# Performance work log

Hardware: AMD Instinct MI355X
Metric: run time of the kernel (lower is better)

## Reference

```python
import jax, jax.numpy as jnp
import numpy as np

N_NODES = 100000
N_EDGES = 1600000
D_IN = 128
D_OUT = 128


def setup_inputs() -> dict:
    key = jax.random.key(0)
    k_x, k_w, k_r, k_c, k_v = jax.random.split(key, 5)
    x = jax.random.normal(k_x, (N_NODES, D_IN), dtype=jnp.float32)
    # xavier_uniform: U(-a, a), a = sqrt(6/(fan_in+fan_out))
    a = float(np.sqrt(6.0 / (D_IN + D_OUT)))
    W = jax.random.uniform(k_w, (D_IN, D_OUT), dtype=jnp.float32, minval=-a, maxval=a)
    edge_row = jax.random.randint(k_r, (N_EDGES,), 0, N_NODES, dtype=jnp.int32)
    edge_col = jax.random.randint(k_c, (N_EDGES,), 0, N_NODES, dtype=jnp.int32)
    edge_val = jax.random.uniform(k_v, (N_EDGES,), dtype=jnp.float32)
    return {"x": x, "W": W, "edge_row": edge_row, "edge_col": edge_col, "edge_val": edge_val}


def reference(x, W, edge_row, edge_col, edge_val):
    # dropout with p=0.0 is the identity (module default), so omitted.
    support = x @ W                                  # [N, D_OUT] dense GEMM
    # sparse adj @ support in COO form: out[r] += v * support[c]
    msgs = support[edge_col] * edge_val[:, None]      # [E, D_OUT] irregular gather
    out = jax.ops.segment_sum(msgs, edge_row, num_segments=x.shape[0])
    return jnp.tanh(out)
```

## Files before the change

kernel.cpp:

```cpp
#include <hip/hip_runtime.h>
#include <hip/hip_bf16.h>
#include <hip/hip_fp16.h>
#include <math.h>

#define D 128
#define BIN_SHIFT 8
#define BIN_ROWS 256
#define NB_MAX 512
#define CPAD 16
#define AW 4096

typedef _Float16 half8 __attribute__((ext_vector_type(8)));
typedef float floatx4 __attribute__((ext_vector_type(4)));
typedef float floatx2 __attribute__((ext_vector_type(2)));

__global__ void gcn_wt_kernel(const float* __restrict__ W,
                              unsigned short* __restrict__ wt,
                              int* __restrict__ cbin) {
    const int i = blockIdx.x * 256 + threadIdx.x;
    const int n = i >> 7, k = i & 127;
    wt[i] = __half_as_ushort(__float2half_rn(W[k * D + n]));
    if (blockIdx.x < 2) cbin[blockIdx.x * 256 + threadIdx.x] = 0;
}

__global__ __launch_bounds__(256) void gcn_gemm_kernel(
        const float* __restrict__ x, const unsigned short* __restrict__ wt,
        unsigned short* __restrict__ support2, int n_nodes) {
    const int wave = threadIdx.x >> 6;
    const int lane = threadIdx.x & 63;
    const int q = lane >> 4;
    const int n16 = lane & 15;
    const int row_base = blockIdx.x * 128 + wave * 32;
    if (row_base >= n_nodes) return;

    const half8* wt8 = (const half8*)wt;

    floatx4 acc[2][8];
#pragma unroll
    for (int mt = 0; mt < 2; ++mt)
#pragma unroll
        for (int nt = 0; nt < 8; ++nt) acc[mt][nt] = (floatx4){0.f, 0.f, 0.f, 0.f};

#pragma unroll
    for (int kc = 0; kc < 4; ++kc) {
        half8 b[8];
#pragma unroll
        for (int nt = 0; nt < 8; ++nt)
            b[nt] = wt8[(nt * 16 + n16) * 16 + kc * 4 + q];
#pragma unroll
        for (int mt = 0; mt < 2; ++mt) {
            const float* xp = x + (size_t)(row_base + mt * 16 + n16) * D
                                + kc * 32 + q * 8;
            const float4 f0 = *(const float4*)xp;
            const float4 f1 = *(const float4*)(xp + 4);
            half8 a;
            a[0] = (_Float16)f0.x; a[1] = (_Float16)f0.y;
            a[2] = (_Float16)f0.z; a[3] = (_Float16)f0.w;
            a[4] = (_Float16)f1.x; a[5] = (_Float16)f1.y;
            a[6] = (_Float16)f1.z; a[7] = (_Float16)f1.w;
#pragma unroll
            for (int nt = 0; nt < 8; ++nt)
                acc[mt][nt] = __builtin_amdgcn_mfma_f32_16x16x32_f16(
                    a, b[nt], acc[mt][nt], 0, 0, 0);
        }
    }

#pragma unroll
    for (int mt = 0; mt < 2; ++mt) {
        const int r0 = row_base + mt * 16 + q * 4;
#pragma unroll
        for (int nt = 0; nt < 8; ++nt) {
            const int col = nt * 16 + n16;
#pragma unroll
            for (int i = 0; i < 4; ++i)
                support2[(size_t)(r0 + i) * D + col] =
                    __half_as_ushort(__float2half_rn(acc[mt][nt][i]));
        }
    }
}

__global__ __launch_bounds__(256) void gcn_chist_kernel(
        const int* __restrict__ erow, int* __restrict__ cbin, int n_edges) {
    __shared__ int h[NB_MAX];
    const int t = threadIdx.x;
    h[t] = 0;
    h[t + 256] = 0;
    __syncthreads();
    const int stride = gridDim.x * 256 * 4;
    const int nv = n_edges & ~3;
    for (int i = (blockIdx.x * 256 + t) * 4; i + 3 < n_edges; i += stride) {
        const int4 r = *(const int4*)(erow + i);
        atomicAdd(&h[r.x >> BIN_SHIFT], 1);
        atomicAdd(&h[r.y >> BIN_SHIFT], 1);
        atomicAdd(&h[r.z >> BIN_SHIFT], 1);
        atomicAdd(&h[r.w >> BIN_SHIFT], 1);
    }
    if (blockIdx.x == 0) {
        for (int i = nv + t; i < n_edges; i += 256)
            atomicAdd(&h[erow[i] >> BIN_SHIFT], 1);
    }
    __syncthreads();
    if (h[t] > 0) atomicAdd(&cbin[t], h[t]);
    if (h[t + 256] > 0) atomicAdd(&cbin[t + 256], h[t + 256]);
}

__global__ __launch_bounds__(512) void gcn_cscan_kernel(
        const int* __restrict__ cbin, int* __restrict__ cbase,
        int* __restrict__ ccur, int* __restrict__ offsets,
        int nbins, int n_nodes, int n_edges) {
    __shared__ int sm[512];
    const int t = threadIdx.x;
    const int v = (t < nbins) ? cbin[t] : 0;
    sm[t] = v;
    __syncthreads();
    for (int off = 1; off < 512; off <<= 1) {
        int tv = (t >= off) ? sm[t - off] : 0;
        __syncthreads();
        sm[t] += tv;
        __syncthreads();
    }
    const int ex = sm[t] - v;
    if (t < nbins) { cbase[t] = ex; ccur[t * CPAD] = ex; }
    if (t == 0) { cbase[nbins] = n_edges; offsets[n_nodes] = n_edges; }
}

__global__ __launch_bounds__(512) void gcn_binA_kernel(
        const int* __restrict__ erow, const int* __restrict__ ecol,
        const float* __restrict__ eval, int* __restrict__ ccur,
        uint2* __restrict__ tmp8, int n_edges, int nbins) {
    __shared__ uint2 recs[AW];
    __shared__ int hist[NB_MAX];
    __shared__ int lstart[NB_MAX];
    __shared__ int gbase[NB_MAX];
    const int t = threadIdx.x;
    const int w0 = blockIdx.x * AW;
    const int wend = min(w0 + AW, n_edges);
    const int cnt = wend - w0;

    hist[t] = 0;
    __syncthreads();

    for (int i = w0 + t; i < wend; i += 512)
        atomicAdd(&hist[erow[i] >> BIN_SHIFT], 1);
    __syncthreads();

    {
        const int v = hist[t];
        gbase[t] = v;
        __syncthreads();
        for (int off = 1; off < 512; off <<= 1) {
            int tv = (t >= off) ? gbase[t - off] : 0;
            __syncthreads();
            gbase[t] += tv;
            __syncthreads();
        }
        lstart[t] = gbase[t] - v;
        __syncthreads();
    }

    {
        const int c = hist[t];
        int gb = 0;
        if (t < nbins && c > 0) gb = atomicAdd(&ccur[t * CPAD], c);
        __syncthreads();
        gbase[t] = gb;
        hist[t] = lstart[t];
    }
    __syncthreads();

    for (int i = w0 + t; i < wend; i += 512) {
        const int r = erow[i];
        const int c = ecol[i];
        const unsigned short vh = __half_as_ushort(__float2half_rn(eval[i]));
        const int b = r >> BIN_SHIFT;
        const int p = atomicAdd(&hist[b], 1);
        recs[p] = make_uint2(((unsigned)r << 15) | vh, (unsigned)c);
    }
    __syncthreads();

    for (int s = t; s < cnt; s += 512) {
        const uint2 rec = recs[s];
        const int b = (int)(rec.x >> 15) >> BIN_SHIFT;
        tmp8[gbase[b] + (s - lstart[b])] = rec;
    }
}

__global__ __launch_bounds__(256) void gcn_binB_kernel(
        const uint2* __restrict__ tmp8, const int* __restrict__ cbase,
        int* __restrict__ offsets,
        unsigned int* __restrict__ rec4, int n_nodes) {
    __shared__ int cnt[BIN_ROWS];
    __shared__ int sm[BIN_ROWS];
    const int bin = blockIdx.x;
    const int r0 = bin << BIN_SHIFT;
    const int t = threadIdx.x;
    cnt[t] = 0;
    __syncthreads();

    const int beg = cbase[bin];
    const int end = cbase[bin + 1];

    for (int i = beg + t; i < end; i += 256)
        atomicAdd(&cnt[(int)(tmp8[i].x >> 15) - r0], 1);
    __syncthreads();

    const int v = cnt[t];
    sm[t] = v;
    __syncthreads();
    for (int off = 1; off < 256; off <<= 1) {
        int tv = (t >= off) ? sm[t - off] : 0;
        __syncthreads();
        sm[t] += tv;
        __syncthreads();
    }
    const int mypos = beg + sm[t] - v;

    const int row = r0 + t;
    if (row < n_nodes) offsets[row] = mypos;
    __syncthreads();
    cnt[t] = mypos;
    __syncthreads();

    for (int i = beg + t; i < end; i += 256) {
        const uint2 p = tmp8[i];
        const int pos = atomicAdd(&cnt[(int)(p.x >> 15) - r0], 1);
        rec4[pos] = (p.y << 15) | (p.x & 0x7FFFu);
    }
}

__global__ __launch_bounds__(256) void gcn_gather_kernel(
        const unsigned int* __restrict__ support_u,
        const unsigned int* __restrict__ rec4,
        const int* __restrict__ offsets,
        float* __restrict__ out, int n_nodes) {
    const int node = __builtin_amdgcn_readfirstlane(
        blockIdx.x * 4 + (threadIdx.x >> 6));
    const int lane = threadIdx.x & 63;
    if (node >= n_nodes) return;

    const int beg = offsets[node];
    const int end = offsets[node + 1];

    float ax = 0.f, ay = 0.f, bx = 0.f, by = 0.f;
    int e = beg;
    for (; e + 7 < end; e += 8) {
        unsigned r[8], s[8];
#pragma unroll
        for (int j = 0; j < 8; ++j) r[j] = rec4[e + j];
#pragma unroll
        for (int j = 0; j < 8; ++j)
            s[j] = support_u[(size_t)(r[j] >> 15) * 64 + lane];
#pragma unroll
        for (int j = 0; j < 8; ++j) {
            const float v = __half2float(__ushort_as_half((unsigned short)(r[j] & 0x7FFFu)));
            const float slo = __half2float(__ushort_as_half((unsigned short)(s[j] & 0xFFFFu)));
            const float shi = __half2float(__ushort_as_half((unsigned short)(s[j] >> 16)));
            if (j & 1) { bx += v * slo; by += v * shi; }
            else       { ax += v * slo; ay += v * shi; }
        }
    }
    for (; e + 3 < end; e += 4) {
        unsigned r[4], s[4];
#pragma unroll
        for (int j = 0; j < 4; ++j) r[j] = rec4[e + j];
#pragma unroll
        for (int j = 0; j < 4; ++j)
            s[j] = support_u[(size_t)(r[j] >> 15) * 64 + lane];
#pragma unroll
        for (int j = 0; j < 4; ++j) {
            const float v = __half2float(__ushort_as_half((unsigned short)(r[j] & 0x7FFFu)));
            const float slo = __half2float(__ushort_as_half((unsigned short)(s[j] & 0xFFFFu)));
            const float shi = __half2float(__ushort_as_half((unsigned short)(s[j] >> 16)));
            if (j & 1) { bx += v * slo; by += v * shi; }
            else       { ax += v * slo; ay += v * shi; }
        }
    }
    for (; e < end; ++e) {
        const unsigned r = rec4[e];
        const unsigned s = support_u[(size_t)(r >> 15) * 64 + lane];
        const float v = __half2float(__ushort_as_half((unsigned short)(r & 0x7FFFu)));
        ax += v * __half2float(__ushort_as_half((unsigned short)(s & 0xFFFFu)));
        ay += v * __half2float(__ushort_as_half((unsigned short)(s >> 16)));
    }

    floatx2 res;
    res.x = tanhf(ax + bx);
    res.y = tanhf(ay + by);
    floatx2* out2 = (floatx2*)out;
    __builtin_nontemporal_store(res, &out2[(size_t)node * 64 + lane]);
}

extern "C" void kernel_launch(void* const* d_in, const int* in_sizes, int n_in,
                              void* d_out, int out_size, void* d_ws, size_t ws_size,
                              hipStream_t stream) {
    const float* x    = (const float*)d_in[0];
    const float* W    = (const float*)d_in[1];
    const int*   erow = (const int*)d_in[2];
    const int*   ecol = (const int*)d_in[3];
    const float* eval = (const float*)d_in[4];
    float* out = (float*)d_out;

    const int n_nodes = in_sizes[0] / D;
    const int n_edges = in_sizes[2];
    const int nbins = (n_nodes + BIN_ROWS - 1) >> BIN_SHIFT;

    unsigned short* support2 = (unsigned short*)d_ws;
    unsigned short* wt = support2 + (size_t)n_nodes * D;
    uint2* tmp8   = (uint2*)(wt + D * D);
    unsigned int* rec4 = (unsigned int*)(tmp8 + n_edges);
    int*  offsets = (int*)(rec4 + n_edges);
    int*  cbin    = offsets + n_nodes + 1;
    int*  cbase   = cbin + NB_MAX;
    int*  ccur    = cbase + NB_MAX + 1;

    gcn_wt_kernel<<<(D * D) / 256, 256, 0, stream>>>(W, wt, cbin);
    gcn_gemm_kernel<<<(n_nodes + 127) / 128, 256, 0, stream>>>(
        x, wt, support2, n_nodes);

    gcn_chist_kernel<<<320, 256, 0, stream>>>(erow, cbin, n_edges);
    gcn_cscan_kernel<<<1, 512, 0, stream>>>(cbin, cbase, ccur, offsets,
                                            nbins, n_nodes, n_edges);

    gcn_binA_kernel<<<(n_edges + AW - 1) / AW, 512, 0, stream>>>(
        erow, ecol, eval, ccur, tmp8, n_edges, nbins);
    gcn_binB_kernel<<<nbins, 256, 0, stream>>>(tmp8, cbase, offsets, rec4, n_nodes);

    gcn_gather_kernel<<<(n_nodes + 3) / 4, 256, 0, stream>>>(
        (const unsigned int*)support2, rec4, offsets, out, n_nodes);
}
```

Before: 241.3 us.

## Fuse W transpose with row histogram and recompute bin scan redundantly per block

```diff
diff --git a/kernel.cpp b/kernel.cpp
--- a/kernel.cpp
+++ b/kernel.cpp
@@ -9,18 +9,48 @@
 #define NB_MAX 512
 #define CPAD 16
 #define AW 4096
+#define CHB 64
 
 typedef _Float16 half8 __attribute__((ext_vector_type(8)));
 typedef float floatx4 __attribute__((ext_vector_type(4)));
 typedef float floatx2 __attribute__((ext_vector_type(2)));
 
-__global__ void gcn_wt_kernel(const float* __restrict__ W,
-                              unsigned short* __restrict__ wt,
-                              int* __restrict__ cbin) {
-    const int i = blockIdx.x * 256 + threadIdx.x;
-    const int n = i >> 7, k = i & 127;
-    wt[i] = __half_as_ushort(__float2half_rn(W[k * D + n]));
-    if (blockIdx.x < 2) cbin[blockIdx.x * 256 + threadIdx.x] = 0;
+__global__ __launch_bounds__(256) void gcn_prep_kernel(
+        const float* __restrict__ W, unsigned short* __restrict__ wt,
+        int* __restrict__ ccur, int* __restrict__ part,
+        int* __restrict__ offsets, const int* __restrict__ erow,
+        int n_nodes, int n_edges) {
+    __shared__ int h[NB_MAX];
+    const int t = threadIdx.x;
+    const int bid = blockIdx.x;
+    const int gi = bid * 256 + t;
+
+    {
+        const int n = gi >> 7, k = gi & 127;
+        wt[gi] = __half_as_ushort(__float2half_rn(W[k * D + n]));
+    }
+    if (gi < NB_MAX * CPAD) ccur[gi] = 0;
+    if (gi == 0) offsets[n_nodes] = n_edges;
+
+    h[t] = 0;
+    h[t + 256] = 0;
+    __syncthreads();
+    const int nv = n_edges & ~3;
+    const int stride = CHB * 256 * 4;
+    for (int i = gi * 4; i + 3 < n_edges; i += stride) {
+        const int4 r = *(const int4*)(erow + i);
+        atomicAdd(&h[r.x >> BIN_SHIFT], 1);
+        atomicAdd(&h[r.y >> BIN_SHIFT], 1);
+        atomicAdd(&h[r.z >> BIN_SHIFT], 1);
+        atomicAdd(&h[r.w >> BIN_SHIFT], 1);
+    }
+    if (bid == 0) {
+        for (int i = nv + t; i < n_edges; i += 256)
+            atomicAdd(&h[erow[i] >> BIN_SHIFT], 1);
+    }
+    __syncthreads();
+    part[bid * NB_MAX + t] = h[t];
+    part[bid * NB_MAX + t + 256] = h[t + 256];
 }
 
 __global__ __launch_bounds__(256) void gcn_gemm_kernel(
@@ -79,56 +109,13 @@
     }
 }
 
-__global__ __launch_bounds__(256) void gcn_chist_kernel(
-        const int* __restrict__ erow, int* __restrict__ cbin, int n_edges) {
-    __shared__ int h[NB_MAX];
-    const int t = threadIdx.x;
-    h[t] = 0;
-    h[t + 256] = 0;
-    __syncthreads();
-    const int stride = gridDim.x * 256 * 4;
-    const int nv = n_edges & ~3;
-    for (int i = (blockIdx.x * 256 + t) * 4; i + 3 < n_edges; i += stride) {
-        const int4 r = *(const int4*)(erow + i);
-        atomicAdd(&h[r.x >> BIN_SHIFT], 1);
-        atomicAdd(&h[r.y >> BIN_SHIFT], 1);
-        atomicAdd(&h[r.z >> BIN_SHIFT], 1);
-        atomicAdd(&h[r.w >> BIN_SHIFT], 1);
-    }
-    if (blockIdx.x == 0) {
-        for (int i = nv + t; i < n_edges; i += 256)
-            atomicAdd(&h[erow[i] >> BIN_SHIFT], 1);
-    }
-    __syncthreads();
-    if (h[t] > 0) atomicAdd(&cbin[t], h[t]);
-    if (h[t + 256] > 0) atomicAdd(&cbin[t + 256], h[t + 256]);
-}
-
-__global__ __launch_bounds__(512) void gcn_cscan_kernel(
-        const int* __restrict__ cbin, int* __restrict__ cbase,
-        int* __restrict__ ccur, int* __restrict__ offsets,
-        int nbins, int n_nodes, int n_edges) {
-    __shared__ int sm[512];
-    const int t = threadIdx.x;
-    const int v = (t < nbins) ? cbin[t] : 0;
-    sm[t] = v;
-    __syncthreads();
-    for (int off = 1; off < 512; off <<= 1) {
-        int tv = (t >= off) ? sm[t - off] : 0;
-        __syncthreads();
-        sm[t] += tv;
-        __syncthreads();
-    }
-    const int ex = sm[t] - v;
-    if (t < nbins) { cbase[t] = ex; ccur[t * CPAD] = ex; }
-    if (t == 0) { cbase[nbins] = n_edges; offsets[n_nodes] = n_edges; }
-}
-
 __global__ __launch_bounds__(512) void gcn_binA_kernel(
         const int* __restrict__ erow, const int* __restrict__ ecol,
-        const float* __restrict__ eval, int* __restrict__ ccur,
-        uint2* __restrict__ tmp8, int n_edges, int nbins) {
+        const float* __restrict__ eval, const int* __restrict__ part,
+        int* __restrict__ ccur, uint2* __restrict__ tmp8,
+        int n_edges, int nbins) {
     __shared__ uint2 recs[AW];
+    __shared__ int cbs[NB_MAX];
     __shared__ int hist[NB_MAX];
     __shared__ int lstart[NB_MAX];
     __shared__ int gbase[NB_MAX];
@@ -137,6 +124,19 @@
     const int wend = min(w0 + AW, n_edges);
     const int cnt = wend - w0;
 
+    int csum = 0;
+#pragma unroll 8
+    for (int k = 0; k < CHB; ++k) csum += part[k * NB_MAX + t];
+    hist[t] = csum;
+    __syncthreads();
+    for (int off = 1; off < 512; off <<= 1) {
+        int tv = (t >= off) ? hist[t - off] : 0;
+        __syncthreads();
+        hist[t] += tv;
+        __syncthreads();
+    }
+    cbs[t] = hist[t] - csum;
+    __syncthreads();
     hist[t] = 0;
     __syncthreads();
 
@@ -161,7 +161,7 @@
     {
         const int c = hist[t];
         int gb = 0;
-        if (t < nbins && c > 0) gb = atomicAdd(&ccur[t * CPAD], c);
+        if (t < nbins && c > 0) gb = cbs[t] + atomicAdd(&ccur[t * CPAD], c);
         __syncthreads();
         gbase[t] = gb;
         hist[t] = lstart[t];
@@ -186,19 +186,44 @@
 }
 
 __global__ __launch_bounds__(256) void gcn_binB_kernel(
-        const uint2* __restrict__ tmp8, const int* __restrict__ cbase,
-        int* __restrict__ offsets,
-        unsigned int* __restrict__ rec4, int n_nodes) {
+        const uint2* __restrict__ tmp8, const int* __restrict__ part,
+        int* __restrict__ offsets, unsigned int* __restrict__ rec4,
+        int n_nodes, int nbins) {
     __shared__ int cnt[BIN_ROWS];
-    __shared__ int sm[BIN_ROWS];
+    __shared__ int sm[256];
+    __shared__ int bb[2];
     const int bin = blockIdx.x;
     const int r0 = bin << BIN_SHIFT;
     const int t = threadIdx.x;
+
+    int s0 = 0, s1 = 0;
+    const int2* p2 = (const int2*)part;
+#pragma unroll 8
+    for (int k = 0; k < CHB; ++k) {
+        const int2 p = p2[k * 256 + t];
+        s0 += p.x; s1 += p.y;
+    }
+    const int s2 = s0 + s1;
+    sm[t] = s2;
+    __syncthreads();
+    for (int off = 1; off < 256; off <<= 1) {
+        int tv = (t >= off) ? sm[t - off] : 0;
+        __syncthreads();
+        sm[t] += tv;
+        __syncthreads();
+    }
+    const int ex = sm[t] - s2;
+    if (2 * t == bin)     bb[0] = ex;
+    if (2 * t + 1 == bin) bb[0] = ex + s0;
+    if (2 * t == bin + 1)     bb[1] = ex;
+    if (2 * t + 1 == bin + 1) bb[1] = ex + s0;
+    if (t == 255 && bin + 1 == NB_MAX) bb[1] = sm[255];
+    __syncthreads();
+    const int beg = bb[0];
+    const int end = bb[1];
+
     cnt[t] = 0;
     __syncthreads();
-
-    const int beg = cbase[bin];
-    const int end = cbase[bin + 1];
 
     for (int i = beg + t; i < end; i += 256)
         atomicAdd(&cnt[(int)(tmp8[i].x >> 15) - r0], 1);
@@ -309,22 +334,17 @@
     uint2* tmp8   = (uint2*)(wt + D * D);
     unsigned int* rec4 = (unsigned int*)(tmp8 + n_edges);
     int*  offsets = (int*)(rec4 + n_edges);
-    int*  cbin    = offsets + n_nodes + 1;
-    int*  cbase   = cbin + NB_MAX;
-    int*  ccur    = cbase + NB_MAX + 1;
-
-    gcn_wt_kernel<<<(D * D) / 256, 256, 0, stream>>>(W, wt, cbin);
+    int*  part    = offsets + n_nodes + 1;
+    int*  ccur    = part + CHB * NB_MAX;
+
+    gcn_prep_kernel<<<CHB, 256, 0, stream>>>(W, wt, ccur, part, offsets,
+                                             erow, n_nodes, n_edges);
     gcn_gemm_kernel<<<(n_nodes + 127) / 128, 256, 0, stream>>>(
         x, wt, support2, n_nodes);
-
-    gcn_chist_kernel<<<320, 256, 0, stream>>>(erow, cbin, n_edges);
-    gcn_cscan_kernel<<<1, 512, 0, stream>>>(cbin, cbase, ccur, offsets,
-                                            nbins, n_nodes, n_edges);
-
     gcn_binA_kernel<<<(n_edges + AW - 1) / AW, 512, 0, stream>>>(
-        erow, ecol, eval, ccur, tmp8, n_edges, nbins);
-    gcn_binB_kernel<<<nbins, 256, 0, stream>>>(tmp8, cbase, offsets, rec4, n_nodes);
-
+        erow, ecol, eval, part, ccur, tmp8, n_edges, nbins);
+    gcn_binB_kernel<<<nbins, 256, 0, stream>>>(tmp8, part, offsets, rec4,
+                                               n_nodes, nbins);
     gcn_gather_kernel<<<(n_nodes + 3) / 4, 256, 0, stream>>>(
         (const unsigned int*)support2, rec4, offsets, out, n_nodes);
 }
```

Measured after the change: 243.9 us. No clear change (+1.1%).
